# Performance work log

Measured on AMD Instinct MI355X. Metric: run time of the kernel, lower is better.

The kernel has to match this reference:

```python
import jax, jax.numpy as jnp
import numpy as np

D_MODEL = 1024
N_HEADS = 16
D_K = D_MODEL // N_HEADS
B, S = 8, 1024
EPS = 1e-8


def setup_inputs() -> dict:
    key = jax.random.key(0)
    ks = jax.random.split(key, 6)
    scale = 1.0 / np.sqrt(D_MODEL)
    return {
        "Q_in": jax.random.normal(ks[0], (B, S, D_MODEL), jnp.float32),
        "mask": jax.random.randint(ks[1], (B, 1, S, S), 0, 2, jnp.int32),
        "Wq": jax.random.normal(ks[2], (D_MODEL, D_MODEL), jnp.float32) * scale,
        "bq": jnp.zeros((D_MODEL,), jnp.float32),
        "Wk": jax.random.normal(ks[3], (D_MODEL, D_MODEL), jnp.float32) * scale,
        "bk": jnp.zeros((D_MODEL,), jnp.float32),
        "Wv": jax.random.normal(ks[4], (D_MODEL, D_MODEL), jnp.float32) * scale,
        "bv": jnp.zeros((D_MODEL,), jnp.float32),
        "Wo": jax.random.normal(ks[5], (D_MODEL, D_MODEL), jnp.float32) * scale,
        "bo": jnp.zeros((D_MODEL,), jnp.float32),
    }


def reference(Q_in, mask, Wq, bq, Wk, bk, Wv, bv, Wo, bo):
    # QKV projections: [B,S,D] -> [B,H,S,d_k]
    def split_heads(x):
        return x.reshape(B, S, N_HEADS, D_K).transpose(0, 2, 1, 3)

    Q = split_heads(Q_in @ Wq + bq)
    K = split_heads(Q_in @ Wk + bk)
    V = split_heads(Q_in @ Wv + bv)

    # scaled scores [B,H,S,S], standard softmax
    scores = jnp.einsum("bhqd,bhkd->bhqk", Q, K) / jnp.sqrt(
        jnp.asarray(D_K, jnp.float32))
    scores = jax.nn.softmax(scores, axis=-1)
    # non-standard: multiplicative mask AFTER softmax, then row renorm
    scores = scores * mask.astype(scores.dtype)
    attn = scores / (jnp.sum(scores, axis=-1, keepdims=True) + EPS)

    context = jnp.einsum("bhqk,bhkd->bhqd", attn, V)
    context = context.transpose(0, 2, 1, 3).reshape(B, S, D_MODEL)
    return context @ Wo + bo
```

## Files before the change

### kernel.cpp

```cpp
#include <hip/hip_runtime.h>
#include <hip/hip_bf16.h>
#include <stdint.h>

typedef __attribute__((ext_vector_type(4))) float f32x4;
typedef __attribute__((ext_vector_type(8))) __bf16 bf16x8;
typedef unsigned short u16;
typedef unsigned int u32;
typedef unsigned long long u64;

#define NH 16
#define DKK 64
#define QSCALE 0.18033688011112042f

__device__ __forceinline__ u16 f2bf(float f) {
    u32 u = __builtin_bit_cast(u32, f);
    u32 r = (u + 0x7fffu + ((u >> 16) & 1u)) >> 16;
    return (u16)r;
}

__device__ __forceinline__ u16 cvt_bf(float f) {
    __hip_bfloat16 h = __float2bfloat16(f);
    return *reinterpret_cast<u16*>(&h);
}

__device__ __forceinline__ float exp2_fast(float x) {
    return __builtin_amdgcn_exp2f(x);
}

__device__ __forceinline__ void gload16(const void* g, void* l) {
    __builtin_amdgcn_global_load_lds((const __attribute__((address_space(1))) void*)g,
                                     (__attribute__((address_space(3))) void*)l, 16, 0, 0);
}

__global__ __launch_bounds__(256) void k_prep(const float* __restrict__ x,
                                              u16* __restrict__ xb,
                                              const float* __restrict__ wq,
                                              const float* __restrict__ wk,
                                              const float* __restrict__ wv,
                                              const float* __restrict__ wo,
                                              u16* __restrict__ wt,
                                              const int* __restrict__ mask,
                                              u64* __restrict__ mb) {
    int bx = blockIdx.x;
    if (bx < 4096) {
        int i = bx * 256 + threadIdx.x;
        const float4* p = (const float4*)x + (size_t)i * 2;
        float4 a = p[0], b = p[1];
        union { u16 h[8]; uint4 q; } o;
        o.h[0] = f2bf(a.x); o.h[1] = f2bf(a.y); o.h[2] = f2bf(a.z); o.h[3] = f2bf(a.w);
        o.h[4] = f2bf(b.x); o.h[5] = f2bf(b.y); o.h[6] = f2bf(b.z); o.h[7] = f2bf(b.w);
        ((uint4*)xb)[i] = o.q;
    } else if (bx < 8192) {
        int idx = bx - 4096;
        int z = idx >> 10;
        const float* w = (z == 0) ? wq : (z == 1) ? wk : (z == 2) ? wv : wo;
        __shared__ float t[32][33];
        int tx = threadIdx.x & 31, ty = threadIdx.x >> 5;
        int n0 = (idx & 31) * 32, k0 = ((idx >> 5) & 31) * 32;
        for (int rr = 0; rr < 4; ++rr)
            t[ty + rr * 8][tx] = w[(size_t)(k0 + ty + rr * 8) * 1024 + n0 + tx];
        __syncthreads();
        for (int rr = 0; rr < 4; ++rr) {
            int n = n0 + ty + rr * 8;
            wt[((size_t)z * 1024 + n) * 1024 + k0 + tx] = f2bf(t[tx][ty + rr * 8]);
        }
    } else {
        int wid = ((bx - 8192) * 256 + threadIdx.x) >> 6;
        int lane = threadIdx.x & 63;
        for (int c = wid; c < 8 * 1024 * 16; c += 8192) {
            int m = mask[(size_t)c * 64 + lane];
            u64 bits = __ballot(m != 0);
            if (lane == 0)
                mb[(c & 0xFFFFC000u) | ((c & 15) << 10) | ((c >> 4) & 1023)] = bits;
        }
    }
}

template <int MODE>
__global__ __launch_bounds__(256) void k_gemm(const u16* __restrict__ A,
                                              const u16* __restrict__ Bt,
                                              const float* __restrict__ b0,
                                              const float* __restrict__ b1,
                                              const float* __restrict__ b2,
                                              u16* __restrict__ q_out,
                                              u16* __restrict__ k_out,
                                              u16* __restrict__ v_out,
                                              float* __restrict__ out) {
    __shared__ u16 As[128 * 64];
    __shared__ u16 Bs[128 * 64];
    int tid = threadIdx.x;
    int wv = tid >> 6, lane = tid & 63;
    int r = lane & 15, g = lane >> 4;
    int wr = wv >> 1, wc = wv & 1;
    int m0 = blockIdx.x * 128, n0 = blockIdx.y * 128;
    f32x4 acc[4][4] = {};
    for (int kt = 0; kt < 1024; kt += 64) {
        __syncthreads();
#pragma unroll
        for (int i = 0; i < 4; ++i) {
            int e = i * 256 + tid;
            int row = e >> 3;
            int cs = ((e & 7) ^ (row & 7)) * 8;
            gload16(A + (size_t)(m0 + row) * 1024 + kt + cs, As + (size_t)e * 8);
            gload16(Bt + (size_t)(n0 + row) * 1024 + kt + cs, Bs + (size_t)e * 8);
        }
        __syncthreads();
#pragma unroll
        for (int half = 0; half < 2; ++half) {
            int gc = g + half * 4;
            bf16x8 aF[4], bF[4];
#pragma unroll
            for (int m = 0; m < 4; ++m) {
                int ro = wr * 64 + m * 16 + r;
                aF[m] = *(const bf16x8*)&As[ro * 64 + ((gc ^ (ro & 7)) << 3)];
            }
#pragma unroll
            for (int n = 0; n < 4; ++n) {
                int ro = wc * 64 + n * 16 + r;
                bF[n] = *(const bf16x8*)&Bs[ro * 64 + ((gc ^ (ro & 7)) << 3)];
            }
#pragma unroll
            for (int m = 0; m < 4; ++m)
#pragma unroll
                for (int n = 0; n < 4; ++n)
                    acc[m][n] = __builtin_amdgcn_mfma_f32_16x16x32_bf16(aF[m], bF[n], acc[m][n], 0, 0, 0);
        }
    }
    for (int m = 0; m < 4; ++m) {
        int rowb = m0 + wr * 64 + m * 16 + 4 * g;
        for (int n = 0; n < 4; ++n) {
            int col = n0 + wc * 64 + n * 16 + r;
            if (MODE == 0) {
                int w = col >> 10, cn = col & 1023;
                const float* bp = (w == 0) ? b0 : (w == 1) ? b1 : b2;
                u16* dst = (w == 0) ? q_out : (w == 1) ? k_out : v_out;
                float sc = (w == 0) ? QSCALE : 1.0f;
                int h = cn >> 6, d = cn & 63;
                float bias = bp[cn];
                for (int i = 0; i < 4; ++i) {
                    int row = rowb + i;
                    int b = row >> 10, s = row & 1023;
                    float v = (acc[m][n][i] + bias) * sc;
                    dst[((size_t)(b * NH + h) * 1024 + s) * 64 + d] = f2bf(v);
                }
            } else {
                float bias = b0[col];
                for (int i = 0; i < 4; ++i) {
                    int row = rowb + i;
                    out[(size_t)row * 1024 + col] = acc[m][n][i] + bias;
                }
            }
        }
    }
}

__global__ __launch_bounds__(256) void k_transpose_v(const u16* __restrict__ vb,
                                                     u16* __restrict__ vt) {
    __shared__ u16 t[64][72];
    int bh = blockIdx.y, s0 = blockIdx.x * 64;
    int tid = threadIdx.x;
    for (int i = 0; i < 2; ++i) {
        int e = i * 256 + tid;
        int row = e >> 3, ch = (e & 7) * 8;
        uint4 v = *(const uint4*)(vb + ((size_t)bh * 1024 + s0 + row) * 64 + ch);
        *(uint4*)&t[row][ch] = v;
    }
    __syncthreads();
    for (int i = 0; i < 2; ++i) {
        int e = i * 256 + tid;
        int d = e >> 3, ch = (e & 7) * 8;
        union { u16 h[8]; uint4 q; } o;
        for (int j = 0; j < 8; ++j) o.h[j] = t[ch + j][d];
        *(uint4*)(vt + ((size_t)bh * 64 + d) * 1024 + s0 + ch) = o.q;
    }
}

__global__ __launch_bounds__(256, 3) void k_attn(const u16* __restrict__ qb,
                                                 const u16* __restrict__ kb,
                                                 const u16* __restrict__ vt,
                                                 const u64* __restrict__ mbits,
                                                 u16* __restrict__ ctx) {
    __shared__ u16 Kd[2][64 * 64];
    __shared__ u16 Vd[2][64 * 64];
    int tid = threadIdx.x, wv = tid >> 6, lane = tid & 63;
    int r = lane & 15, g = lane >> 4;
    int q0 = blockIdx.x * 128, bh = blockIdx.y;
    int b = bh >> 4, h = bh & 15;

    bf16x8 aq[2][2];
#pragma unroll
    for (int qg = 0; qg < 2; ++qg) {
        const u16* qp = qb + ((size_t)bh * 1024 + q0 + wv * 32 + qg * 16 + r) * 64 + g * 8;
        aq[qg][0] = *(const bf16x8*)qp;
        aq[qg][1] = *(const bf16x8*)(qp + 32);
    }

    f32x4 of[2][4] = {};
    f32x4 zacc[2] = {};
    const bf16x8 vone = {(__bf16)1.f, (__bf16)1.f, (__bf16)1.f, (__bf16)1.f,
                         (__bf16)1.f, (__bf16)1.f, (__bf16)1.f, (__bf16)1.f};

    const u64* mrow = mbits + ((size_t)b * 16) * 1024 + q0 + wv * 32 + r;
    u64 mbc[2] = {mrow[0], mrow[16]};

    for (int i2 = 0; i2 < 2; ++i2) {
        int e = i2 * 256 + tid;
        int s = e >> 3, c = e & 7;
        int cs = (c ^ (s & 7)) * 8;
        int kr = (s & 0x20) | ((s & 0x0C) << 1) | ((s & 0x10) >> 2) | (s & 3);
        gload16(kb + ((size_t)bh * 1024 + kr) * 64 + cs, Kd[0] + (size_t)e * 8);
        gload16(vt + ((size_t)bh * 64 + s) * 1024 + cs, Vd[0] + (size_t)e * 8);
    }
    __syncthreads();

    for (int t = 0; t < 16; ++t) {
        int cur = t & 1;
        u64 mbn0 = 0, mbn1 = 0;
        if (t < 15) {
            int ktn = (t + 1) * 64;
            for (int i2 = 0; i2 < 2; ++i2) {
                int e = i2 * 256 + tid;
                int s = e >> 3, c = e & 7;
                int cs = (c ^ (s & 7)) * 8;
                int kr = (s & 0x20) | ((s & 0x0C) << 1) | ((s & 0x10) >> 2) | (s & 3);
                gload16(kb + ((size_t)bh * 1024 + ktn + kr) * 64 + cs, Kd[cur ^ 1] + (size_t)e * 8);
                gload16(vt + ((size_t)bh * 64 + s) * 1024 + ktn + cs, Vd[cur ^ 1] + (size_t)e * 8);
            }
            mbn0 = mrow[(size_t)(t + 1) * 1024];
            mbn1 = mrow[(size_t)(t + 1) * 1024 + 16];
        }
        const u16* K = Kd[cur];
        const u16* V = Vd[cur];

        bf16x8 bk0[4], bk1[4];
#pragma unroll
        for (int nf = 0; nf < 4; ++nf) {
            int rowk = (nf * 16 + r) * 64;
            bk0[nf] = *(const bf16x8*)&K[rowk + ((g ^ (r & 7)) << 3)];
            bk1[nf] = *(const bf16x8*)&K[rowk + (((g + 4) ^ (r & 7)) << 3)];
        }

        bf16x8 pfr[2][2];
#pragma unroll
        for (int qg = 0; qg < 2; ++qg) {
            f32x4 sf[4];
            __builtin_amdgcn_s_setprio(1);
#pragma unroll
            for (int nf = 0; nf < 4; ++nf) {
                f32x4 z = {0.f, 0.f, 0.f, 0.f};
                z = __builtin_amdgcn_mfma_f32_16x16x32_bf16(bk0[nf], aq[qg][0], z, 0, 0, 0);
                sf[nf] = __builtin_amdgcn_mfma_f32_16x16x32_bf16(bk1[nf], aq[qg][1], z, 0, 0, 0);
            }
            __builtin_amdgcn_s_setprio(0);
            u64 m64 = mbc[qg] >> (g * 8);
            u32 mlo = (u32)m64, mhi = (u32)(m64 >> 32);
            u32 pw[8];
#pragma unroll
            for (int nf = 0; nf < 4; ++nf) {
                u32 nib = ((nf & 2) ? mhi : mlo) >> ((nf & 1) * 4);
                u32 pm0 = ((nib & 1) ? 0xFFFFu : 0u) | ((nib & 2) ? 0xFFFF0000u : 0u);
                u32 pm1 = ((nib & 4) ? 0xFFFFu : 0u) | ((nib & 8) ? 0xFFFF0000u : 0u);
                float e0 = exp2_fast(sf[nf][0]), e1 = exp2_fast(sf[nf][1]);
                float e2 = exp2_fast(sf[nf][2]), e3 = exp2_fast(sf[nf][3]);
                pw[2 * nf]     = (((u32)cvt_bf(e0)) | ((u32)cvt_bf(e1) << 16)) & pm0;
                pw[2 * nf + 1] = (((u32)cvt_bf(e2)) | ((u32)cvt_bf(e3) << 16)) & pm1;
            }
            union { u32 w[4]; bf16x8 v; } f0, f1;
            f0.w[0] = pw[0]; f0.w[1] = pw[1]; f0.w[2] = pw[2]; f0.w[3] = pw[3];
            f1.w[0] = pw[4]; f1.w[1] = pw[5]; f1.w[2] = pw[6]; f1.w[3] = pw[7];
            pfr[qg][0] = f0.v;
            pfr[qg][1] = f1.v;
            __builtin_amdgcn_s_setprio(1);
            zacc[qg] = __builtin_amdgcn_mfma_f32_16x16x32_bf16(vone, pfr[qg][0], zacc[qg], 0, 0, 0);
            zacc[qg] = __builtin_amdgcn_mfma_f32_16x16x32_bf16(vone, pfr[qg][1], zacc[qg], 0, 0, 0);
            __builtin_amdgcn_s_setprio(0);
        }
        __builtin_amdgcn_s_setprio(1);
#pragma unroll
        for (int ks = 0; ks < 2; ++ks) {
#pragma unroll
            for (int nf = 0; nf < 4; ++nf) {
                bf16x8 av = *(const bf16x8*)&V[(nf * 16 + r) * 64 + (((ks * 4 + g) ^ (r & 7)) << 3)];
                of[0][nf] = __builtin_amdgcn_mfma_f32_16x16x32_bf16(av, pfr[0][ks], of[0][nf], 0, 0, 0);
                of[1][nf] = __builtin_amdgcn_mfma_f32_16x16x32_bf16(av, pfr[1][ks], of[1][nf], 0, 0, 0);
            }
        }
        __builtin_amdgcn_s_setprio(0);
        mbc[0] = mbn0;
        mbc[1] = mbn1;
        __syncthreads();
    }

#pragma unroll
    for (int qg = 0; qg < 2; ++qg) {
        float inv = 1.0f / zacc[qg][0];
        int qrow = q0 + wv * 32 + qg * 16 + r;
        u16* crow = ctx + ((size_t)(b * 1024 + qrow)) * 1024 + h * 64;
#pragma unroll
        for (int nf = 0; nf < 4; ++nf) {
            u32 w0 = ((u32)cvt_bf(of[qg][nf][0] * inv)) | ((u32)cvt_bf(of[qg][nf][1] * inv) << 16);
            u32 w1 = ((u32)cvt_bf(of[qg][nf][2] * inv)) | ((u32)cvt_bf(of[qg][nf][3] * inv) << 16);
            *(u32*)(crow + nf * 16 + g * 4) = w0;
            *(u32*)(crow + nf * 16 + g * 4 + 2) = w1;
        }
    }
}

extern "C" void kernel_launch(void* const* d_in, const int* in_sizes, int n_in,
                              void* d_out, int out_size, void* d_ws, size_t ws_size,
                              hipStream_t stream) {
    const float* Q_in = (const float*)d_in[0];
    const int*   mask = (const int*)d_in[1];
    const float* Wq = (const float*)d_in[2];
    const float* bq = (const float*)d_in[3];
    const float* Wk = (const float*)d_in[4];
    const float* bk = (const float*)d_in[5];
    const float* Wv = (const float*)d_in[6];
    const float* bv = (const float*)d_in[7];
    const float* Wo = (const float*)d_in[8];
    const float* bo = (const float*)d_in[9];

    char* ws = (char*)d_ws;
    u16* Xb = (u16*)(ws);
    u16* Wt = (u16*)(ws + 16777216);
    u16* Qb = (u16*)(ws + 25165824);
    u16* Kb = (u16*)(ws + 41943040);
    u16* Vb = (u16*)(ws + 58720256);
    u16* Vt = (u16*)(ws + 75497472);
    u64* Mb = (u64*)(ws + 92274688);
    u16* Ctx = Vb;

    k_prep<<<10240, 256, 0, stream>>>(Q_in, Xb, Wq, Wk, Wv, Wo, Wt, mask, Mb);
    k_gemm<0><<<dim3(64, 24), 256, 0, stream>>>(Xb, Wt, bq, bk, bv, Qb, Kb, Vb, nullptr);
    k_transpose_v<<<dim3(16, 128), 256, 0, stream>>>(Vb, Vt);
    k_attn<<<dim3(8, 128), 256, 0, stream>>>(Qb, Kb, Vt, Mb, Ctx);
    k_gemm<1><<<dim3(64, 8), 256, 0, stream>>>(Ctx, Wt + (size_t)3 * 1024 * 1024,
                                               bo, nullptr, nullptr,
                                               nullptr, nullptr, nullptr, (float*)d_out);
}
```

Measured before the change: 175.4 us.

## Use 256x256 double-buffered GEMM tiles with 512 threads and prefetch

Rewrites the bf16 GEMM kernel used for the QKV and output projections. It now uses 256x256 output tiles, 8 waves per block and double-buffered LDS, loading the next K-slice while MFMAs run on the current one. MFMA phases are bracketed by barriers and s_setprio to interleave waves. The larger tiles shrink the grids to 384 and 128 blocks. That may leave many CUs idle on the output projection and lower occupancy, since each block uses 128KB of LDS.

```diff
diff --git a/kernel.cpp b/kernel.cpp
--- a/kernel.cpp
+++ b/kernel.cpp
@@ -77,59 +77,89 @@
 }
 
 template <int MODE>
-__global__ __launch_bounds__(256) void k_gemm(const u16* __restrict__ A,
-                                              const u16* __restrict__ Bt,
-                                              const float* __restrict__ b0,
-                                              const float* __restrict__ b1,
-                                              const float* __restrict__ b2,
-                                              u16* __restrict__ q_out,
-                                              u16* __restrict__ k_out,
-                                              u16* __restrict__ v_out,
-                                              float* __restrict__ out) {
-    __shared__ u16 As[128 * 64];
-    __shared__ u16 Bs[128 * 64];
+__global__ __launch_bounds__(512, 2) void k_gemm(const u16* __restrict__ A,
+                                                 const u16* __restrict__ Bt,
+                                                 const float* __restrict__ b0,
+                                                 const float* __restrict__ b1,
+                                                 const float* __restrict__ b2,
+                                                 u16* __restrict__ q_out,
+                                                 u16* __restrict__ k_out,
+                                                 u16* __restrict__ v_out,
+                                                 float* __restrict__ out) {
+    __shared__ u16 As[2][256 * 64];
+    __shared__ u16 Bs[2][256 * 64];
     int tid = threadIdx.x;
     int wv = tid >> 6, lane = tid & 63;
     int r = lane & 15, g = lane >> 4;
-    int wr = wv >> 1, wc = wv & 1;
-    int m0 = blockIdx.x * 128, n0 = blockIdx.y * 128;
-    f32x4 acc[4][4] = {};
-    for (int kt = 0; kt < 1024; kt += 64) {
-        __syncthreads();
-#pragma unroll
-        for (int i = 0; i < 4; ++i) {
-            int e = i * 256 + tid;
-            int row = e >> 3;
-            int cs = ((e & 7) ^ (row & 7)) * 8;
-            gload16(A + (size_t)(m0 + row) * 1024 + kt + cs, As + (size_t)e * 8);
-            gload16(Bt + (size_t)(n0 + row) * 1024 + kt + cs, Bs + (size_t)e * 8);
-        }
-        __syncthreads();
-#pragma unroll
-        for (int half = 0; half < 2; ++half) {
-            int gc = g + half * 4;
-            bf16x8 aF[4], bF[4];
-#pragma unroll
-            for (int m = 0; m < 4; ++m) {
-                int ro = wr * 64 + m * 16 + r;
-                aF[m] = *(const bf16x8*)&As[ro * 64 + ((gc ^ (ro & 7)) << 3)];
-            }
-#pragma unroll
-            for (int n = 0; n < 4; ++n) {
-                int ro = wc * 64 + n * 16 + r;
-                bF[n] = *(const bf16x8*)&Bs[ro * 64 + ((gc ^ (ro & 7)) << 3)];
-            }
-#pragma unroll
-            for (int m = 0; m < 4; ++m)
-#pragma unroll
-                for (int n = 0; n < 4; ++n)
-                    acc[m][n] = __builtin_amdgcn_mfma_f32_16x16x32_bf16(aF[m], bF[n], acc[m][n], 0, 0, 0);
-        }
-    }
-    for (int m = 0; m < 4; ++m) {
-        int rowb = m0 + wr * 64 + m * 16 + 4 * g;
-        for (int n = 0; n < 4; ++n) {
-            int col = n0 + wc * 64 + n * 16 + r;
+    int wr = wv >> 2, wc = wv & 3;
+    int m0 = blockIdx.x * 256, n0 = blockIdx.y * 256;
+    f32x4 acc[8][4] = {};
+
+    const u16* ga[4];
+    const u16* gb[4];
+#pragma unroll
+    for (int i = 0; i < 4; ++i) {
+        int e = i * 512 + tid;
+        int row = e >> 3;
+        int cs = ((e & 7) ^ (row & 7)) * 8;
+        ga[i] = A + (size_t)(m0 + row) * 1024 + cs;
+        gb[i] = Bt + (size_t)(n0 + row) * 1024 + cs;
+    }
+
+#define GSTAGE(slot, kt)                                                        \
+    do {                                                                        \
+        for (int i_ = 0; i_ < 4; ++i_) {                                        \
+            gload16(ga[i_] + (kt), As[slot] + (size_t)(i_ * 512 + tid) * 8);    \
+            gload16(gb[i_] + (kt), Bs[slot] + (size_t)(i_ * 512 + tid) * 8);    \
+        }                                                                       \
+    } while (0)
+
+    GSTAGE(0, 0);
+    asm volatile("s_waitcnt vmcnt(0)" ::: "memory");
+    __builtin_amdgcn_s_barrier();
+
+    for (int t = 0; t < 16; ++t) {
+        int cur = t & 1;
+        if (t < 15) GSTAGE(cur ^ 1, (t + 1) * 64);
+        const u16* RA = As[cur];
+        const u16* RB = Bs[cur];
+#pragma unroll
+        for (int p = 0; p < 4; ++p) {
+            int mh = p >> 1, nh = p & 1;
+            bf16x8 aF[2][4], bF[2][2];
+#pragma unroll
+            for (int kk = 0; kk < 2; ++kk) {
+                int ck = ((kk * 4 + g) ^ (r & 7)) << 3;
+#pragma unroll
+                for (int mf = 0; mf < 4; ++mf)
+                    aF[kk][mf] = *(const bf16x8*)&RA[(wr * 128 + mh * 64 + mf * 16 + r) * 64 + ck];
+#pragma unroll
+                for (int nf = 0; nf < 2; ++nf)
+                    bF[kk][nf] = *(const bf16x8*)&RB[(wc * 64 + nh * 32 + nf * 16 + r) * 64 + ck];
+            }
+            __builtin_amdgcn_s_barrier();
+            __builtin_amdgcn_s_setprio(1);
+#pragma unroll
+            for (int kk = 0; kk < 2; ++kk)
+#pragma unroll
+                for (int mf = 0; mf < 4; ++mf)
+#pragma unroll
+                    for (int nf = 0; nf < 2; ++nf)
+                        acc[mh * 4 + mf][nh * 2 + nf] =
+                            __builtin_amdgcn_mfma_f32_16x16x32_bf16(
+                                aF[kk][mf], bF[kk][nf], acc[mh * 4 + mf][nh * 2 + nf], 0, 0, 0);
+            __builtin_amdgcn_s_setprio(0);
+            __builtin_amdgcn_s_barrier();
+        }
+        if (t < 15) asm volatile("s_waitcnt vmcnt(0)" ::: "memory");
+        __builtin_amdgcn_s_barrier();
+    }
+#undef GSTAGE
+
+    for (int mi = 0; mi < 8; ++mi) {
+        int rowb = m0 + wr * 128 + mi * 16 + 4 * g;
+        for (int ni = 0; ni < 4; ++ni) {
+            int col = n0 + wc * 64 + ni * 16 + r;
             if (MODE == 0) {
                 int w = col >> 10, cn = col & 1023;
                 const float* bp = (w == 0) ? b0 : (w == 1) ? b1 : b2;
@@ -140,14 +170,14 @@
                 for (int i = 0; i < 4; ++i) {
                     int row = rowb + i;
                     int b = row >> 10, s = row & 1023;
-                    float v = (acc[m][n][i] + bias) * sc;
+                    float v = (acc[mi][ni][i] + bias) * sc;
                     dst[((size_t)(b * NH + h) * 1024 + s) * 64 + d] = f2bf(v);
                 }
             } else {
                 float bias = b0[col];
                 for (int i = 0; i < 4; ++i) {
                     int row = rowb + i;
-                    out[(size_t)row * 1024 + col] = acc[m][n][i] + bias;
+                    out[(size_t)row * 1024 + col] = acc[mi][ni][i] + bias;
                 }
             }
         }
@@ -331,10 +361,10 @@
     u16* Ctx = Vb;
 
     k_prep<<<10240, 256, 0, stream>>>(Q_in, Xb, Wq, Wk, Wv, Wo, Wt, mask, Mb);
-    k_gemm<0><<<dim3(64, 24), 256, 0, stream>>>(Xb, Wt, bq, bk, bv, Qb, Kb, Vb, nullptr);
+    k_gemm<0><<<dim3(32, 12), 512, 0, stream>>>(Xb, Wt, bq, bk, bv, Qb, Kb, Vb, nullptr);
     k_transpose_v<<<dim3(16, 128), 256, 0, stream>>>(Vb, Vt);
     k_attn<<<dim3(8, 128), 256, 0, stream>>>(Qb, Kb, Vt, Mb, Ctx);
-    k_gemm<1><<<dim3(64, 8), 256, 0, stream>>>(Ctx, Wt + (size_t)3 * 1024 * 1024,
+    k_gemm<1><<<dim3(32, 4), 512, 0, stream>>>(Ctx, Wt + (size_t)3 * 1024 * 1024,
                                                bo, nullptr, nullptr,
                                                nullptr, nullptr, nullptr, (float*)d_out);
 }
```

Measured after the change: 218.7 us. 1.25x slower.
